# Performance work log

Measured on AMD Instinct MI355X. Metric: run time of the kernel, lower is better.

Reference implementation:

```python
import math
import jax, jax.numpy as jnp
import numpy as np

NHEAD = 16
LN_EPS = 1e-5


def _layernorm(x, g, b):
    mu = jnp.mean(x, axis=-1, keepdims=True)
    var = jnp.mean((x - mu) ** 2, axis=-1, keepdims=True)
    return (x - mu) * jax.lax.rsqrt(var + LN_EPS) * g + b


def setup_inputs() -> dict:
    key = jax.random.key(0)
    ks = jax.random.split(key, 12)
    S, B, D, V, L = 512, 8, 1024, 32000, 6
    w = 0.02
    return {
        "src": jax.random.randint(ks[0], (S, B), 0, V),
        "emb_table": jax.random.uniform(ks[1], (V, D), jnp.float32, -0.1, 0.1),
        "embed_mean": jax.random.normal(ks[2], (D, D), jnp.float32) * (1.0 / math.sqrt(D + 1)),
        "qkv_w": jax.random.normal(ks[3], (L, 3 * D, D), jnp.float32) * w,
        "qkv_b": jnp.zeros((L, 3 * D), jnp.float32),
        "o_w": jax.random.normal(ks[4], (L, D, D), jnp.float32) * w,
        "o_b": jnp.zeros((L, D), jnp.float32),
        "w1": jax.random.normal(ks[5], (L, D, D), jnp.float32) * w,
        "b1": jnp.zeros((L, D), jnp.float32),
        "w2": jax.random.normal(ks[6], (L, D, D), jnp.float32) * w,
        "b2": jnp.zeros((L, D), jnp.float32),
        "ln1_g": jnp.ones((L, D), jnp.float32),
        "ln1_b": jnp.zeros((L, D), jnp.float32),
        "ln2_g": jnp.ones((L, D), jnp.float32),
        "ln2_b": jnp.zeros((L, D), jnp.float32),
        "dec_w": jax.random.uniform(ks[7], (V, D), jnp.float32, -0.1, 0.1),
        "dec_b": jnp.zeros((V,), jnp.float32),
    }


def reference(src, emb_table, embed_mean, qkv_w, qkv_b, o_w, o_b,
              w1, b1, w2, b2, ln1_g, ln1_b, ln2_g, ln2_b, dec_w, dec_b):
    S, B = src.shape
    D = emb_table.shape[1]
    L = qkv_w.shape[0]
    HD = D // NHEAD

    # embedding * sqrt(d_model), then Bayesian embed linear (eval: diff = 0)
    x = emb_table[src] * jnp.asarray(math.sqrt(D), x_dtype := emb_table.dtype)  # [S,B,D]
    x = x @ embed_mean.T

    # sinusoidal positional encoding (interleaved sin/cos)
    pos = jnp.arange(S, dtype=jnp.float32)[:, None]                 # [S,1]
    div = jnp.exp(jnp.arange(0, D, 2, dtype=jnp.float32) * (-math.log(10000.0) / D))
    pe = jnp.stack([jnp.sin(pos * div), jnp.cos(pos * div)], axis=-1).reshape(S, D)
    x = x + pe[:, None, :].astype(x.dtype)

    # causal additive mask [S,S]: 0 on/below diag, -inf above
    mask = jnp.where(jnp.tril(jnp.ones((S, S), bool)), 0.0, -jnp.inf).astype(x.dtype)

    scale = HD ** -0.5
    for l in range(L):
        qkv = x @ qkv_w[l].T + qkv_b[l]                              # [S,B,3D]
        q, k, v = jnp.split(qkv, 3, axis=-1)
        qh = (q * scale).reshape(S, B, NHEAD, HD)
        kh = k.reshape(S, B, NHEAD, HD)
        vh = v.reshape(S, B, NHEAD, HD)
        scores = jnp.einsum('sbhd,tbhd->bhst', qh, kh) + mask        # [B,H,S,S]
        p = jax.nn.softmax(scores, axis=-1)
        att = jnp.einsum('bhst,tbhd->sbhd', p, vh).reshape(S, B, D)
        att = att @ o_w[l].T + o_b[l]
        x = _layernorm(x + att, ln1_g[l], ln1_b[l])
        ff = jax.nn.relu(x @ w1[l].T + b1[l]) @ w2[l].T + b2[l]
        x = _layernorm(x + ff, ln2_g[l], ln2_b[l])

    pred = x @ embed_mean                                            # F.linear(out, embed_mean.T)
    logits = pred @ dec_w.T + dec_b                                  # [S,B,V]
    return logits
```

## Files before the change

kernel.cpp:

```cpp
#include <hip/hip_runtime.h>
#include <stdint.h>

typedef unsigned short u16;
typedef __bf16 bf16x8 __attribute__((ext_vector_type(8)));
typedef float f32x4 __attribute__((ext_vector_type(4)));

#define AS1 __attribute__((address_space(1)))
#define AS3 __attribute__((address_space(3)))

static constexpr int S = 512, Bb = 8, D = 1024, V = 32000, L = 6, NH = 16, HD = 64;
static constexpr int N = S * Bb;
static constexpr int D3 = 3 * D;

__device__ __forceinline__ u16 f2bf(float f) {
  union { float f; uint32_t u; } c; c.f = f;
  uint32_t r = c.u + 0x7FFFu + ((c.u >> 16) & 1u);
  return (u16)(r >> 16);
}

__device__ __forceinline__ float bf2f(u16 u) {
  union { uint32_t i; float f; } c; c.i = ((uint32_t)u) << 16; return c.f;
}

__device__ __forceinline__ void gload16(const void* g, void* l) {
  __builtin_amdgcn_global_load_lds((const AS1 void*)g, (AS3 void*)l, 16, 0, 0);
}

__global__ __launch_bounds__(256) void cvt_kernel(const float* __restrict__ in,
                                                  u16* __restrict__ out, int n4) {
  int idx = blockIdx.x * 256 + threadIdx.x;
  if (idx < n4) {
    float4 v = ((const float4*)in)[idx];
    ushort4 o;
    o.x = f2bf(v.x); o.y = f2bf(v.y); o.z = f2bf(v.z); o.w = f2bf(v.w);
    ((ushort4*)out)[idx] = o;
  }
}

__global__ __launch_bounds__(256) void cvt4_kernel(const float* __restrict__ s0, const float* __restrict__ s1,
                                                   const float* __restrict__ s2, const float* __restrict__ s3,
                                                   u16* __restrict__ d0, u16* __restrict__ d1,
                                                   u16* __restrict__ d2, u16* __restrict__ d3,
                                                   int n0, int n1, int n2) {
  int j = blockIdx.x * 256 + threadIdx.x;
  const float* s; u16* d;
  if (j < n0) { s = s0; d = d0; }
  else {
    j -= n0;
    if (j < n1) { s = s1; d = d1; }
    else {
      j -= n1;
      if (j < n2) { s = s2; d = d2; }
      else { j -= n2; s = s3; d = d3; }
    }
  }
  float4 v = ((const float4*)s)[j];
  ushort4 o;
  o.x = f2bf(v.x); o.y = f2bf(v.y); o.z = f2bf(v.z); o.w = f2bf(v.w);
  ((ushort4*)d)[j] = o;
}

__global__ __launch_bounds__(256) void transpose_cvt(const float* __restrict__ in,
                                                     u16* __restrict__ out) {
  __shared__ float t[32][33];
  const int bx = blockIdx.x * 32, by = blockIdx.y * 32;
  const int tid = threadIdx.x;
  const int c = tid & 31;
#pragma unroll
  for (int r = tid >> 5; r < 32; r += 8)
    t[r][c] = in[(size_t)(by + r) * D + bx + c];
  __syncthreads();
#pragma unroll
  for (int r = tid >> 5; r < 32; r += 8)
    out[(size_t)(bx + r) * D + by + c] = f2bf(t[c][r]);
}

__global__ __launch_bounds__(256) void gather_kernel(const int* __restrict__ src,
                                                     const float* __restrict__ emb,
                                                     u16* __restrict__ xe) {
  int idx = blockIdx.x * 256 + threadIdx.x;
  int n = idx >> 8, d4 = (idx & 255) * 4;
  int tok = src[n];
  float4 v = *(const float4*)(emb + (size_t)tok * D + d4);
  ushort4 o;
  o.x = f2bf(v.x * 32.f); o.y = f2bf(v.y * 32.f);
  o.z = f2bf(v.z * 32.f); o.w = f2bf(v.w * 32.f);
  *(ushort4*)(xe + (size_t)n * D + d4) = o;
}

__global__ __launch_bounds__(256) void ln_kernel(const float* __restrict__ xold,
                                                 const u16* __restrict__ delta,
                                                 const float* __restrict__ g,
                                                 const float* __restrict__ bb,
                                                 float* __restrict__ xnew,
                                                 u16* __restrict__ xbf) {
  const int row = blockIdx.x * 4 + (threadIdx.x >> 6);
  const int lane = threadIdx.x & 63;
  const float* xr = xold + (size_t)row * D;
  const u16* dr = delta + (size_t)row * D;
  float v[16];
  float s = 0.f;
#pragma unroll
  for (int j = 0; j < 16; ++j) { v[j] = xr[j * 64 + lane] + bf2f(dr[j * 64 + lane]); s += v[j]; }
  for (int off = 32; off; off >>= 1) s += __shfl_xor(s, off);
  float mu = s * (1.f / 1024.f);
  float s2 = 0.f;
#pragma unroll
  for (int j = 0; j < 16; ++j) { float dd = v[j] - mu; s2 += dd * dd; }
  for (int off = 32; off; off >>= 1) s2 += __shfl_xor(s2, off);
  float rstd = rsqrtf(s2 * (1.f / 1024.f) + 1e-5f);
#pragma unroll
  for (int j = 0; j < 16; ++j) {
    int c = j * 64 + lane;
    float y = (v[j] - mu) * rstd * g[c] + bb[c];
    xnew[(size_t)row * D + c] = y;
    xbf[(size_t)row * D + c] = f2bf(y);
  }
}

__global__ __launch_bounds__(256) void vtrans_kernel(const u16* __restrict__ qkv,
                                                     u16* __restrict__ vtg) {
  __shared__ u16 t[64][72];
  const int st = blockIdx.x * 64;
  const int bh = blockIdx.y;
  const int b = bh >> 4, h = bh & 15;
  const int tid = threadIdx.x;
#pragma unroll
  for (int r = 0; r < 4; ++r) {
    int l = r * 1024 + tid * 4;
    int s = l >> 6, d = l & 63;
    ushort4 v = *(const ushort4*)(qkv + (size_t)((st + s) * Bb + b) * D3 + 2 * D + h * HD + d);
    *(ushort4*)&t[s][d] = v;
  }
  __syncthreads();
  u16* o = vtg + (size_t)bh * (HD * S) + st;
#pragma unroll
  for (int r = 0; r < 4; ++r) {
    int l = r * 1024 + tid * 4;
    int d = l >> 6, s = l & 63;
    ushort4 v;
    v.x = t[s][d]; v.y = t[s + 1][d]; v.z = t[s + 2][d]; v.w = t[s + 3][d];
    *(ushort4*)(o + (size_t)d * S + s) = v;
  }
}

template <int EPI, bool OBF>
__global__ __launch_bounds__(256) void gemm64(const u16* __restrict__ A,
                                              const u16* __restrict__ B,
                                              const float* __restrict__ bias,
                                              void* __restrict__ Cout,
                                              void* __restrict__ Cout2,
                                              int M, int K) {
  __shared__ u16 lA[4096];
  __shared__ u16 lB[4096];
  const int tid = threadIdx.x;
  const int lane = tid & 63;
  const int w = tid >> 6;
  const int wm = w >> 1, wn = w & 1;
  const int l15 = lane & 15, l4 = lane >> 4;
  const int row0 = blockIdx.y * 64, col0 = blockIdx.x * 64;

  const int sfl = tid * 8;
  const int srow = sfl >> 6;
  const int scol = sfl & 63;
  const u16* Ag = A + (size_t)(row0 + srow) * K + scol;
  const u16* Bg = B + (size_t)(col0 + srow) * K + scol;

  f32x4 acc[2][2] = {};

  for (int kt = 0; kt < K; kt += 64) {
#pragma unroll
    for (int r = 0; r < 2; ++r)
      gload16(Ag + (size_t)r * 32 * K + kt, &lA[r * 2048 + sfl]);
#pragma unroll
    for (int r = 0; r < 2; ++r)
      gload16(Bg + (size_t)r * 32 * K + kt, &lB[r * 2048 + sfl]);
    asm volatile("s_waitcnt vmcnt(0)" ::: "memory");
    __syncthreads();
#pragma unroll
    for (int kk = 0; kk < 2; ++kk) {
      bf16x8 af[2], bfr[2];
#pragma unroll
      for (int i = 0; i < 2; ++i)
        af[i] = *(const bf16x8*)&lA[(wm * 32 + i * 16 + l15) * 64 + kk * 32 + l4 * 8];
#pragma unroll
      for (int j = 0; j < 2; ++j)
        bfr[j] = *(const bf16x8*)&lB[(wn * 32 + j * 16 + l15) * 64 + kk * 32 + l4 * 8];
#pragma unroll
      for (int i = 0; i < 2; ++i)
#pragma unroll
        for (int j = 0; j < 2; ++j)
          acc[i][j] = __builtin_amdgcn_mfma_f32_16x16x32_bf16(af[i], bfr[j], acc[i][j], 0, 0, 0);
    }
    __syncthreads();
  }

#pragma unroll
  for (int i = 0; i < 2; ++i) {
    const int rb = row0 + wm * 32 + i * 16 + l4 * 4;
#pragma unroll
    for (int j = 0; j < 2; ++j) {
      const int c = col0 + wn * 32 + j * 16 + l15;
      float bv = 0.f;
      if constexpr (EPI == 1 || EPI == 2) bv = bias[c];
      float freq = 0.f;
      if constexpr (EPI == 3)
        freq = __expf(-(float)(c & ~1) * (9.210340371976184f / 1024.f));
#pragma unroll
      for (int q = 0; q < 4; ++q) {
        float v = acc[i][j][q] + bv;
        if constexpr (EPI == 2) v = fmaxf(v, 0.f);
        size_t o = (size_t)(rb + q) * M + c;
        if constexpr (EPI == 3) {
          int s = (rb + q) >> 3;
          float a = (float)s * freq;
          float p = (c & 1) ? __cosf(a) : __sinf(a);
          v += p;
          ((float*)Cout)[o] = v;
          ((u16*)Cout2)[o] = f2bf(v);
        } else if constexpr (OBF) {
          ((u16*)Cout)[o] = f2bf(v);
        } else {
          ((float*)Cout)[o] = v;
        }
      }
    }
  }
}

__device__ __forceinline__ void stageA256(const u16* __restrict__ A, u16* __restrict__ ldsA,
                                          int q, int row0, int K, int kt, int w, int lane) {
  const int ls = lane & 7, lr = lane >> 3;
  const int gs = (ls ^ lr) * 8;
#pragma unroll
  for (int i = 0; i < 2; ++i) {
    int rb = q * 8 + w + i * 16;
    int row = rb * 8 + lr;
    gload16(A + (size_t)(row0 + row) * K + kt + gs, ldsA + row * 64 + ls * 8);
  }
}

__device__ __forceinline__ void stageB256(const u16* __restrict__ B, u16* __restrict__ ldsB,
                                          int q, int col0, int K, int kt, int w, int lane) {
  const int ls = lane & 7, lr = lane >> 3;
  const int gs = (ls ^ lr) * 8;
#pragma unroll
  for (int i = 0; i < 2; ++i) {
    int cb = q * 4 + (w & 3) + (w >> 2) * 8 + i * 16;
    int col = cb * 8 + lr;
    gload16(B + (size_t)(col0 + col) * K + kt + gs, ldsB + col * 64 + ls * 8);
  }
}

template <int EPI, bool OBF>
__global__ __launch_bounds__(512, 2) void gemm256(const u16* __restrict__ A,
                                                  const u16* __restrict__ B,
                                                  const float* __restrict__ bias,
                                                  void* __restrict__ Cout,
                                                  int M, int K) {
  __shared__ u16 lds[65536];
  const int tid = threadIdx.x;
  const int w = tid >> 6, lane = tid & 63;
  const int wm = w >> 2, wn = w & 3;
  const int l15 = lane & 15, l4 = lane >> 4;

  const int nwg = gridDim.x;
  const int cpx = nwg >> 3;
  const int f = blockIdx.x;
  const int swz = (f & 7) * cpx + (f >> 3);
  const int GX = M >> 8;
  const int per = 8 * GX;
  const int g = swz / per, r = swz % per;
  const int by = g * 8 + (r & 7);
  const int bx = r >> 3;
  const int row0 = by * 256, col0 = bx * 256;

  const int NT = K >> 6;

  f32x4 acc[8][4] = {};
  bf16x8 af[4][2], b0[2][2], b1[2][2];

  const int sw0 = ((0 * 4 + l4) ^ (l15 & 7)) * 8;
  const int sw1 = ((1 * 4 + l4) ^ (l15 & 7)) * 8;

  {
    u16* A0 = lds;             u16* B0l = lds + 16384;
    u16* A1 = lds + 32768;     u16* B1l = lds + 49152;
    stageA256(A, A0, 0, row0, K, 0, w, lane);
    stageB256(B, B0l, 0, col0, K, 0, w, lane);
    stageB256(B, B0l, 1, col0, K, 0, w, lane);
    stageA256(A, A0, 1, row0, K, 0, w, lane);
    if (NT > 1) {
      stageA256(A, A1, 0, row0, K, 64, w, lane);
      stageB256(B, B1l, 0, col0, K, 64, w, lane);
      stageB256(B, B1l, 1, col0, K, 64, w, lane);
      stageA256(A, A1, 1, row0, K, 64, w, lane);
      asm volatile("s_waitcnt vmcnt(8)" ::: "memory");
    } else {
      asm volatile("s_waitcnt vmcnt(0)" ::: "memory");
    }
    __builtin_amdgcn_s_barrier();
  }

  for (int t = 0; t < NT; ++t) {
    const int cur = t & 1;
    u16* LA = lds + cur * 32768;
    u16* LB = LA + 16384;
    const bool pf = (t + 2 < NT);
    const int kpf = (t + 2) * 64;

#pragma unroll
    for (int mf = 0; mf < 4; ++mf) {
      int row = wm * 128 + mf * 16 + l15;
      af[mf][0] = *(const bf16x8*)&LA[row * 64 + sw0];
      af[mf][1] = *(const bf16x8*)&LA[row * 64 + sw1];
    }
#pragma unroll
    for (int nf = 0; nf < 2; ++nf) {
      int col = wn * 64 + nf * 16 + l15;
      b0[nf][0] = *(const bf16x8*)&LB[col * 64 + sw0];
      b0[nf][1] = *(const bf16x8*)&LB[col * 64 + sw1];
    }
    asm volatile("s_waitcnt lgkmcnt(8)" ::: "memory");
    __builtin_amdgcn_s_barrier();
    asm volatile("s_waitcnt lgkmcnt(0)" ::: "memory");
    __builtin_amdgcn_sched_barrier(0);
    __builtin_amdgcn_s_setprio(1);
#pragma unroll
    for (int mf = 0; mf < 4; ++mf)
#pragma unroll
      for (int nf = 0; nf < 2; ++nf)
#pragma unroll
        for (int ks = 0; ks < 2; ++ks)
          acc[mf][nf] = __builtin_amdgcn_mfma_f32_16x16x32_bf16(af[mf][ks], b0[nf][ks], acc[mf][nf], 0, 0, 0);
    __builtin_amdgcn_s_setprio(0);
    __builtin_amdgcn_s_barrier();

#pragma unroll
    for (int nf = 0; nf < 2; ++nf) {
      int col = wn * 64 + 32 + nf * 16 + l15;
      b1[nf][0] = *(const bf16x8*)&LB[col * 64 + sw0];
      b1[nf][1] = *(const bf16x8*)&LB[col * 64 + sw1];
    }
    if (pf) stageA256(A, LA, 0, row0, K, kpf, w, lane);
    __builtin_amdgcn_s_barrier();
    asm volatile("s_waitcnt lgkmcnt(0)" ::: "memory");
    __builtin_amdgcn_sched_barrier(0);
    __builtin_amdgcn_s_setprio(1);
#pragma unroll
    for (int mf = 0; mf < 4; ++mf)
#pragma unroll
      for (int nf = 0; nf < 2; ++nf)
#pragma unroll
        for (int ks = 0; ks < 2; ++ks)
          acc[mf][2 + nf] = __builtin_amdgcn_mfma_f32_16x16x32_bf16(af[mf][ks], b1[nf][ks], acc[mf][2 + nf], 0, 0, 0);
    __builtin_amdgcn_s_setprio(0);
    __builtin_amdgcn_s_barrier();

#pragma unroll
    for (int mf = 0; mf < 4; ++mf) {
      int row = wm * 128 + 64 + mf * 16 + l15;
      af[mf][0] = *(const bf16x8*)&LA[row * 64 + sw0];
      af[mf][1] = *(const bf16x8*)&LA[row * 64 + sw1];
    }
    if (pf) stageB256(B, LB, 0, col0, K, kpf, w, lane);
    __builtin_amdgcn_s_barrier();
    asm volatile("s_waitcnt lgkmcnt(0)" ::: "memory");
    __builtin_amdgcn_sched_barrier(0);
    __builtin_amdgcn_s_setprio(1);
#pragma unroll
    for (int mf = 0; mf < 4; ++mf)
#pragma unroll
      for (int nf = 0; nf < 2; ++nf)
#pragma unroll
        for (int ks = 0; ks < 2; ++ks)
          acc[4 + mf][nf] = __builtin_amdgcn_mfma_f32_16x16x32_bf16(af[mf][ks], b0[nf][ks], acc[4 + mf][nf], 0, 0, 0);
    __builtin_amdgcn_s_setprio(0);
    __builtin_amdgcn_s_barrier();

    if (pf) {
      stageB256(B, LB, 1, col0, K, kpf, w, lane);
      stageA256(A, LA, 1, row0, K, kpf, w, lane);
    }
    __builtin_amdgcn_s_setprio(1);
#pragma unroll
    for (int mf = 0; mf < 4; ++mf)
#pragma unroll
      for (int nf = 0; nf < 2; ++nf)
#pragma unroll
        for (int ks = 0; ks < 2; ++ks)
          acc[4 + mf][2 + nf] = __builtin_amdgcn_mfma_f32_16x16x32_bf16(af[mf][ks], b1[nf][ks], acc[4 + mf][2 + nf], 0, 0, 0);
    __builtin_amdgcn_s_setprio(0);
    if (pf)               asm volatile("s_waitcnt vmcnt(8)" ::: "memory");
    else if (t + 1 < NT)  asm volatile("s_waitcnt vmcnt(0)" ::: "memory");
    __builtin_amdgcn_s_barrier();
  }

#pragma unroll
  for (int mf = 0; mf < 8; ++mf) {
    const int rb = row0 + wm * 128 + mf * 16 + l4 * 4;
#pragma unroll
    for (int nf = 0; nf < 4; ++nf) {
      const int c = col0 + wn * 64 + nf * 16 + l15;
      float bv = 0.f;
      if constexpr (EPI >= 1) bv = bias[c];
#pragma unroll
      for (int q = 0; q < 4; ++q) {
        float v = acc[mf][nf][q] + bv;
        size_t o = (size_t)(rb + q) * M + c;
        if constexpr (OBF) ((u16*)Cout)[o] = f2bf(v);
        else ((float*)Cout)[o] = v;
      }
    }
  }
}

__global__ __launch_bounds__(256, 1) void attn_kernel(const u16* __restrict__ qkv,
                                                      const u16* __restrict__ vtg,
                                                      u16* __restrict__ att) {
  __shared__ u16 Kl[S * HD];
  __shared__ u16 Vt[HD * S];
  __shared__ u16 Pl[4][32 * 64];
  const int tid = threadIdx.x, lane = tid & 63, w = tid >> 6;
  const int qt = blockIdx.x, h = blockIdx.y, b = blockIdx.z;
  const int l15 = lane & 15, l4 = lane >> 4;

  const int nkv = (qt >= 2) ? 512 : (128 << qt);
  const int sh = (qt == 0) ? 4 : (qt == 1) ? 5 : 6;

  {
    const int sfl = tid * 8;
    for (int r = 0; r < (qt + 1) * 4; ++r) {
      int l = r * 2048 + sfl;
      int s = l >> 6;
      int slot = (l & 63) >> 3;
      int d = (slot ^ (s & 7)) << 3;
      gload16(qkv + (size_t)(s * Bb + b) * D3 + D + h * HD + d, &Kl[l]);
    }
    const u16* vg = vtg + (size_t)(b * NH + h) * (HD * S);
    const int cpr_m1 = (nkv >> 3) - 1;
    for (int r = 0; r < (nkv >> 5); ++r) {
      int c = r * 256 + tid;
      int d = c >> sh, s8 = c & cpr_m1;
      int ss = (s8 ^ (d & 7)) << 3;
      gload16(vg + (size_t)d * S + ss, &Vt[c * 8]);
    }
  }
  asm volatile("s_waitcnt vmcnt(0)" ::: "memory");
  __syncthreads();

  const int qbase = qt * 128 + w * 32;
  bf16x8 qf[2][2];
#pragma unroll
  for (int fm = 0; fm < 2; ++fm)
#pragma unroll
    for (int kk = 0; kk < 2; ++kk) {
      int qs = qbase + fm * 16 + l15;
      qf[fm][kk] = *(const bf16x8*)(qkv + (size_t)(qs * Bb + b) * D3 + h * HD + kk * 32 + l4 * 8);
    }

  const int sw0 = ((0 * 4 + l4) ^ (l15 & 7)) * 8;
  const int sw1 = ((1 * 4 + l4) ^ (l15 & 7)) * 8;

  float lsum[2][4];
  f32x4 o[2][4] = {};
#pragma unroll
  for (int fm = 0; fm < 2; ++fm)
#pragma unroll
    for (int j = 0; j < 4; ++j) lsum[fm][j] = 0.f;

  const int nchunk = qbase / 64 + 1;
  for (int ch = 0; ch < nchunk; ++ch) {
    f32x4 sc[2][4] = {};
#pragma unroll
    for (int kk = 0; kk < 2; ++kk) {
      bf16x8 kb[4];
#pragma unroll
      for (int fn = 0; fn < 4; ++fn)
        kb[fn] = *(const bf16x8*)&Kl[(ch * 64 + fn * 16 + l15) * 64 + (kk ? sw1 : sw0)];
#pragma unroll
      for (int fm = 0; fm < 2; ++fm)
#pragma unroll
        for (int fn = 0; fn < 4; ++fn)
          sc[fm][fn] = __builtin_amdgcn_mfma_f32_16x16x32_bf16(qf[fm][kk], kb[fn], sc[fm][fn], 0, 0, 0);
    }
    const bool mk = (ch == nchunk - 1);
    u16* P = &Pl[w][0];
#pragma unroll
    for (int fm = 0; fm < 2; ++fm)
#pragma unroll
      for (int j = 0; j < 4; ++j) {
        const int rlow = l4 * 4 + j;
        const int q_s = qbase + fm * 16 + rlow;
        const int cswz = (rlow & 7) << 3;
#pragma unroll
        for (int fn = 0; fn < 4; ++fn) {
          float p = __expf(sc[fm][fn][j] * 0.125f);
          if (mk) {
            int k_s = ch * 64 + fn * 16 + l15;
            if (k_s > q_s) p = 0.f;
          }
          lsum[fm][j] += p;
          P[(fm * 16 + rlow) * 64 + ((fn * 16 + l15) ^ cswz)] = f2bf(p);
        }
      }
    asm volatile("" ::: "memory");
#pragma unroll
    for (int kk = 0; kk < 2; ++kk) {
      bf16x8 pa[2];
#pragma unroll
      for (int fm = 0; fm < 2; ++fm)
        pa[fm] = *(const bf16x8*)&P[(fm * 16 + l15) * 64 + ((kk * 32 + l4 * 8) ^ ((l15 & 7) << 3))];
#pragma unroll
      for (int fd = 0; fd < 4; ++fd) {
        bf16x8 vb = *(const bf16x8*)&Vt[(fd * 16 + l15) * nkv + (((ch * 8 + kk * 4 + l4) ^ (l15 & 7)) << 3)];
#pragma unroll
        for (int fm = 0; fm < 2; ++fm)
          o[fm][fd] = __builtin_amdgcn_mfma_f32_16x16x32_bf16(pa[fm], vb, o[fm][fd], 0, 0, 0);
      }
    }
    asm volatile("" ::: "memory");
  }
  for (int off = 1; off <= 8; off <<= 1)
#pragma unroll
    for (int fm = 0; fm < 2; ++fm)
#pragma unroll
      for (int j = 0; j < 4; ++j)
        lsum[fm][j] += __shfl_xor(lsum[fm][j], off);
#pragma unroll
  for (int fm = 0; fm < 2; ++fm)
#pragma unroll
    for (int fd = 0; fd < 4; ++fd)
#pragma unroll
      for (int j = 0; j < 4; ++j) {
        int s = qbase + fm * 16 + l4 * 4 + j;
        int d = h * HD + fd * 16 + l15;
        att[(size_t)(s * Bb + b) * D + d] = f2bf(o[fm][fd][j] / lsum[fm][j]);
      }
}

extern "C" void kernel_launch(void* const* d_in, const int* in_sizes, int n_in,
                              void* d_out, int out_size, void* d_ws, size_t ws_size,
                              hipStream_t stream) {
  const int* src = (const int*)d_in[0];
  const float* emb = (const float*)d_in[1];
  const float* em = (const float*)d_in[2];
  const float* qkvw = (const float*)d_in[3];
  const float* qkvb = (const float*)d_in[4];
  const float* ow = (const float*)d_in[5];
  const float* ob = (const float*)d_in[6];
  const float* w1 = (const float*)d_in[7];
  const float* b1 = (const float*)d_in[8];
  const float* w2 = (const float*)d_in[9];
  const float* b2 = (const float*)d_in[10];
  const float* ln1g = (const float*)d_in[11];
  const float* ln1b = (const float*)d_in[12];
  const float* ln2g = (const float*)d_in[13];
  const float* ln2b = (const float*)d_in[14];
  const float* decw = (const float*)d_in[15];
  const float* decb = (const float*)d_in[16];
  float* out = (float*)d_out;

  uint8_t* ws = (uint8_t*)d_ws;
  size_t off = 0;
  auto alloc = [&](size_t bytes) -> void* {
    void* p = ws + off;
    off += (bytes + 255) & ~(size_t)255;
    return p;
  };
  u16* decw_bf = (u16*)alloc((size_t)V * D * 2);
  u16* lw_qkv  = (u16*)alloc((size_t)D3 * D * 2);
  u16* lw_o    = (u16*)alloc((size_t)D * D * 2);
  u16* lw_1    = (u16*)alloc((size_t)D * D * 2);
  u16* lw_2    = (u16*)alloc((size_t)D * D * 2);
  u16* em_bf   = (u16*)alloc((size_t)D * D * 2);
  u16* emT_bf  = (u16*)alloc((size_t)D * D * 2);
  u16* xe_bf   = (u16*)alloc((size_t)N * D * 2);
  float* x_f   = (float*)alloc((size_t)N * D * 4);
  u16* x_bf    = (u16*)alloc((size_t)N * D * 2);
  u16* tmp_bf  = (u16*)alloc((size_t)N * D * 2);
  u16* qkv_bf  = (u16*)alloc((size_t)N * D3 * 2);
  u16* vtg     = (u16*)alloc((size_t)N * D * 2);
  u16* att_bf  = (u16*)alloc((size_t)N * D * 2);
  u16* h_bf    = (u16*)alloc((size_t)N * D * 2);
  u16* pred_bf = (u16*)alloc((size_t)N * D * 2);
  (void)ws_size; (void)in_sizes; (void)n_in; (void)out_size;

  cvt_kernel<<<1024, 256, 0, stream>>>(em, em_bf, D * D / 4);
  transpose_cvt<<<dim3(32, 32), 256, 0, stream>>>(em, emT_bf);
  gather_kernel<<<N * D / 1024, 256, 0, stream>>>(src, emb, xe_bf);
  gemm64<3, false><<<dim3(D / 64, N / 64), 256, 0, stream>>>(xe_bf, em_bf, nullptr, x_f, x_bf, D, D);

  const int nqkv4 = D3 * D / 4;
  const int ndd4 = D * D / 4;
  for (int l = 0; l < L; ++l) {
    cvt4_kernel<<<(nqkv4 + 3 * ndd4) / 256, 256, 0, stream>>>(
        qkvw + (size_t)l * D3 * D, ow + (size_t)l * D * D,
        w1 + (size_t)l * D * D, w2 + (size_t)l * D * D,
        lw_qkv, lw_o, lw_1, lw_2, nqkv4, ndd4, ndd4);

    gemm256<1, true><<<(D3 / 256) * (N / 256), 512, 0, stream>>>(x_bf, lw_qkv, qkvb + l * D3, qkv_bf, D3, D);
    vtrans_kernel<<<dim3(S / 64, Bb * NH), 256, 0, stream>>>(qkv_bf, vtg);
    attn_kernel<<<dim3(S / 128, NH, Bb), 256, 0, stream>>>(qkv_bf, vtg, att_bf);
    gemm64<1, true><<<dim3(D / 64, N / 64), 256, 0, stream>>>(att_bf, lw_o, ob + l * D, tmp_bf, nullptr, D, D);
    ln_kernel<<<N / 4, 256, 0, stream>>>(x_f, tmp_bf, ln1g + l * D, ln1b + l * D, x_f, x_bf);
    gemm64<2, true><<<dim3(D / 64, N / 64), 256, 0, stream>>>(x_bf, lw_1, b1 + l * D, h_bf, nullptr, D, D);
    gemm64<1, true><<<dim3(D / 64, N / 64), 256, 0, stream>>>(h_bf, lw_2, b2 + l * D, tmp_bf, nullptr, D, D);
    ln_kernel<<<N / 4, 256, 0, stream>>>(x_f, tmp_bf, ln2g + l * D, ln2b + l * D, x_f, x_bf);
  }

  gemm64<0, true><<<dim3(D / 64, N / 64), 256, 0, stream>>>(x_bf, emT_bf, nullptr, pred_bf, nullptr, D, D);
  cvt_kernel<<<(size_t)V * D / 1024, 256, 0, stream>>>(decw, decw_bf, V * D / 4);
  gemm256<1, false><<<(V / 256) * (N / 256), 512, 0, stream>>>(pred_bf, decw_bf, decb, out, V, D);
}
```

Measured before the change: 1.326 ms.

## Stream attention K/V in 256-key halves for two blocks per CU; vectorize layernorm

The attention kernel now loads K and V^T into LDS in two 256-key halves instead of the full 512 keys. This roughly halves shared memory per block, so launch bounds can allow two blocks per CU and raise occupancy. The cost is an extra barrier and reload phase for the later query tiles, with no overlap between load and compute. The layernorm kernel also switches to float4/ushort4 vectorized loads and stores.

After: 1.290 ms. 2.7% less time.

```diff
diff --git a/kernel.cpp b/kernel.cpp
--- a/kernel.cpp
+++ b/kernel.cpp
@@ -96,12 +96,20 @@
                                                  u16* __restrict__ xbf) {
   const int row = blockIdx.x * 4 + (threadIdx.x >> 6);
   const int lane = threadIdx.x & 63;
-  const float* xr = xold + (size_t)row * D;
-  const u16* dr = delta + (size_t)row * D;
+  const float4* xr = (const float4*)(xold + (size_t)row * D);
+  const ushort4* dr = (const ushort4*)(delta + (size_t)row * D);
   float v[16];
   float s = 0.f;
 #pragma unroll
-  for (int j = 0; j < 16; ++j) { v[j] = xr[j * 64 + lane] + bf2f(dr[j * 64 + lane]); s += v[j]; }
+  for (int j = 0; j < 4; ++j) {
+    float4 xv = xr[j * 64 + lane];
+    ushort4 dv = dr[j * 64 + lane];
+    v[4 * j + 0] = xv.x + bf2f(dv.x);
+    v[4 * j + 1] = xv.y + bf2f(dv.y);
+    v[4 * j + 2] = xv.z + bf2f(dv.z);
+    v[4 * j + 3] = xv.w + bf2f(dv.w);
+    s += v[4 * j] + v[4 * j + 1] + v[4 * j + 2] + v[4 * j + 3];
+  }
   for (int off = 32; off; off >>= 1) s += __shfl_xor(s, off);
   float mu = s * (1.f / 1024.f);
   float s2 = 0.f;
@@ -109,12 +117,22 @@
   for (int j = 0; j < 16; ++j) { float dd = v[j] - mu; s2 += dd * dd; }
   for (int off = 32; off; off >>= 1) s2 += __shfl_xor(s2, off);
   float rstd = rsqrtf(s2 * (1.f / 1024.f) + 1e-5f);
-#pragma unroll
-  for (int j = 0; j < 16; ++j) {
-    int c = j * 64 + lane;
-    float y = (v[j] - mu) * rstd * g[c] + bb[c];
-    xnew[(size_t)row * D + c] = y;
-    xbf[(size_t)row * D + c] = f2bf(y);
+  float4* xo = (float4*)(xnew + (size_t)row * D);
+  ushort4* bo = (ushort4*)(xbf + (size_t)row * D);
+#pragma unroll
+  for (int j = 0; j < 4; ++j) {
+    int c4 = j * 64 + lane;
+    float4 gv = ((const float4*)g)[c4];
+    float4 bv = ((const float4*)bb)[c4];
+    float4 y;
+    y.x = (v[4 * j + 0] - mu) * rstd * gv.x + bv.x;
+    y.y = (v[4 * j + 1] - mu) * rstd * gv.y + bv.y;
+    y.z = (v[4 * j + 2] - mu) * rstd * gv.z + bv.z;
+    y.w = (v[4 * j + 3] - mu) * rstd * gv.w + bv.w;
+    xo[c4] = y;
+    ushort4 ob;
+    ob.x = f2bf(y.x); ob.y = f2bf(y.y); ob.z = f2bf(y.z); ob.w = f2bf(y.w);
+    bo[c4] = ob;
   }
 }
 
@@ -415,40 +433,16 @@
   }
 }
 
-__global__ __launch_bounds__(256, 1) void attn_kernel(const u16* __restrict__ qkv,
+__global__ __launch_bounds__(256, 2) void attn_kernel(const u16* __restrict__ qkv,
                                                       const u16* __restrict__ vtg,
                                                       u16* __restrict__ att) {
-  __shared__ u16 Kl[S * HD];
-  __shared__ u16 Vt[HD * S];
+  __shared__ u16 Kl[256 * 64];
+  __shared__ u16 Vt[64 * 256];
   __shared__ u16 Pl[4][32 * 64];
   const int tid = threadIdx.x, lane = tid & 63, w = tid >> 6;
   const int qt = blockIdx.x, h = blockIdx.y, b = blockIdx.z;
   const int l15 = lane & 15, l4 = lane >> 4;
 
-  const int nkv = (qt >= 2) ? 512 : (128 << qt);
-  const int sh = (qt == 0) ? 4 : (qt == 1) ? 5 : 6;
-
-  {
-    const int sfl = tid * 8;
-    for (int r = 0; r < (qt + 1) * 4; ++r) {
-      int l = r * 2048 + sfl;
-      int s = l >> 6;
-      int slot = (l & 63) >> 3;
-      int d = (slot ^ (s & 7)) << 3;
-      gload16(qkv + (size_t)(s * Bb + b) * D3 + D + h * HD + d, &Kl[l]);
-    }
-    const u16* vg = vtg + (size_t)(b * NH + h) * (HD * S);
-    const int cpr_m1 = (nkv >> 3) - 1;
-    for (int r = 0; r < (nkv >> 5); ++r) {
-      int c = r * 256 + tid;
-      int d = c >> sh, s8 = c & cpr_m1;
-      int ss = (s8 ^ (d & 7)) << 3;
-      gload16(vg + (size_t)d * S + ss, &Vt[c * 8]);
-    }
-  }
-  asm volatile("s_waitcnt vmcnt(0)" ::: "memory");
-  __syncthreads();
-
   const int qbase = qt * 128 + w * 32;
   bf16x8 qf[2][2];
 #pragma unroll
@@ -470,56 +464,86 @@
     for (int j = 0; j < 4; ++j) lsum[fm][j] = 0.f;
 
   const int nchunk = qbase / 64 + 1;
-  for (int ch = 0; ch < nchunk; ++ch) {
-    f32x4 sc[2][4] = {};
-#pragma unroll
-    for (int kk = 0; kk < 2; ++kk) {
-      bf16x8 kb[4];
-#pragma unroll
-      for (int fn = 0; fn < 4; ++fn)
-        kb[fn] = *(const bf16x8*)&Kl[(ch * 64 + fn * 16 + l15) * 64 + (kk ? sw1 : sw0)];
+  const int nhalf = (qt >= 2) ? 2 : 1;
+  const u16* vg = vtg + (size_t)(b * NH + h) * (HD * S);
+
+  for (int hf = 0; hf < nhalf; ++hf) {
+    if (hf) __syncthreads();
+    {
+      const int sfl = tid * 8;
+#pragma unroll
+      for (int r = 0; r < 8; ++r) {
+        int l = r * 2048 + sfl;
+        int sl = l >> 6;
+        int slot = (l & 63) >> 3;
+        int d = (slot ^ (sl & 7)) << 3;
+        gload16(qkv + (size_t)((hf * 256 + sl) * Bb + b) * D3 + D + h * HD + d, &Kl[l]);
+      }
+#pragma unroll
+      for (int r = 0; r < 8; ++r) {
+        int c = r * 256 + tid;
+        int d = c >> 5, s8 = c & 31;
+        int ss = (s8 ^ (d & 7)) << 3;
+        gload16(vg + (size_t)d * S + hf * 256 + ss, &Vt[c * 8]);
+      }
+    }
+    asm volatile("s_waitcnt vmcnt(0)" ::: "memory");
+    __syncthreads();
+
+    const int c0 = hf * 4;
+    const int c1 = (nchunk < c0 + 4) ? nchunk : (c0 + 4);
+    for (int ch = c0; ch < c1; ++ch) {
+      const int lc = ch - c0;
+      f32x4 sc[2][4] = {};
+#pragma unroll
+      for (int kk = 0; kk < 2; ++kk) {
+        bf16x8 kb[4];
+#pragma unroll
+        for (int fn = 0; fn < 4; ++fn)
+          kb[fn] = *(const bf16x8*)&Kl[(lc * 64 + fn * 16 + l15) * 64 + (kk ? sw1 : sw0)];
+#pragma unroll
+        for (int fm = 0; fm < 2; ++fm)
+#pragma unroll
+          for (int fn = 0; fn < 4; ++fn)
+            sc[fm][fn] = __builtin_amdgcn_mfma_f32_16x16x32_bf16(qf[fm][kk], kb[fn], sc[fm][fn], 0, 0, 0);
+      }
+      const bool mk = (ch == nchunk - 1);
+      u16* P = &Pl[w][0];
 #pragma unroll
       for (int fm = 0; fm < 2; ++fm)
 #pragma unroll
-        for (int fn = 0; fn < 4; ++fn)
-          sc[fm][fn] = __builtin_amdgcn_mfma_f32_16x16x32_bf16(qf[fm][kk], kb[fn], sc[fm][fn], 0, 0, 0);
-    }
-    const bool mk = (ch == nchunk - 1);
-    u16* P = &Pl[w][0];
-#pragma unroll
-    for (int fm = 0; fm < 2; ++fm)
-#pragma unroll
-      for (int j = 0; j < 4; ++j) {
-        const int rlow = l4 * 4 + j;
-        const int q_s = qbase + fm * 16 + rlow;
-        const int cswz = (rlow & 7) << 3;
-#pragma unroll
-        for (int fn = 0; fn < 4; ++fn) {
-          float p = __expf(sc[fm][fn][j] * 0.125f);
-          if (mk) {
-            int k_s = ch * 64 + fn * 16 + l15;
-            if (k_s > q_s) p = 0.f;
+        for (int j = 0; j < 4; ++j) {
+          const int rlow = l4 * 4 + j;
+          const int q_s = qbase + fm * 16 + rlow;
+          const int cswz = (rlow & 7) << 3;
+#pragma unroll
+          for (int fn = 0; fn < 4; ++fn) {
+            float p = __expf(sc[fm][fn][j] * 0.125f);
+            if (mk) {
+              int k_s = ch * 64 + fn * 16 + l15;
+              if (k_s > q_s) p = 0.f;
+            }
+            lsum[fm][j] += p;
+            P[(fm * 16 + rlow) * 64 + ((fn * 16 + l15) ^ cswz)] = f2bf(p);
           }
-          lsum[fm][j] += p;
-          P[(fm * 16 + rlow) * 64 + ((fn * 16 + l15) ^ cswz)] = f2bf(p);
+        }
+      asm volatile("" ::: "memory");
+#pragma unroll
+      for (int kk = 0; kk < 2; ++kk) {
+        bf16x8 pa[2];
+#pragma unroll
+        for (int fm = 0; fm < 2; ++fm)
+          pa[fm] = *(const bf16x8*)&P[(fm * 16 + l15) * 64 + ((kk * 32 + l4 * 8) ^ ((l15 & 7) << 3))];
+#pragma unroll
+        for (int fd = 0; fd < 4; ++fd) {
+          bf16x8 vb = *(const bf16x8*)&Vt[(fd * 16 + l15) * 256 + (((lc * 8 + kk * 4 + l4) ^ (l15 & 7)) << 3)];
+#pragma unroll
+          for (int fm = 0; fm < 2; ++fm)
+            o[fm][fd] = __builtin_amdgcn_mfma_f32_16x16x32_bf16(pa[fm], vb, o[fm][fd], 0, 0, 0);
         }
       }
-    asm volatile("" ::: "memory");
-#pragma unroll
-    for (int kk = 0; kk < 2; ++kk) {
-      bf16x8 pa[2];
-#pragma unroll
-      for (int fm = 0; fm < 2; ++fm)
-        pa[fm] = *(const bf16x8*)&P[(fm * 16 + l15) * 64 + ((kk * 32 + l4 * 8) ^ ((l15 & 7) << 3))];
-#pragma unroll
-      for (int fd = 0; fd < 4; ++fd) {
-        bf16x8 vb = *(const bf16x8*)&Vt[(fd * 16 + l15) * nkv + (((ch * 8 + kk * 4 + l4) ^ (l15 & 7)) << 3)];
-#pragma unroll
-        for (int fm = 0; fm < 2; ++fm)
-          o[fm][fd] = __builtin_amdgcn_mfma_f32_16x16x32_bf16(pa[fm], vb, o[fm][fd], 0, 0, 0);
-      }
-    }
-    asm volatile("" ::: "memory");
+      asm volatile("" ::: "memory");
+    }
   }
   for (int off = 1; off <= 8; off <<= 1)
 #pragma unroll
```
